# Performance work log

Hardware: AMD Instinct MI355X
Metric: run time of the kernel (lower is better)

Reference implementation:

```python
import jax, jax.numpy as jnp
import numpy as np

OUT, IN = 4096, 4096      # weight_shape
VDIM = 8                  # codebook vector_dim
CODEBOOK_SIZE = 256
LEVEL = 2                 # haar_decomposition_level
INV_SQRT2 = 0.7071067811865476


def unpack_bool(packed, shape):
    # packed: int array of bytes (values 0..255); unpack 8 bits per byte (LSB first)
    bits = (packed[:, None] >> jnp.arange(8, dtype=packed.dtype)) & 1  # [n_bytes, 8]
    return bits.reshape(shape)


def inverse_haar(c, level):
    # c: [..., n] orthonormal Haar coefficients laid out [a_L, d_L, d_{L-1}, ..., d_1]
    n = c.shape[-1]
    m = n >> level
    a = c[..., :m]
    while m < n:
        d = c[..., m:2 * m]
        even = (a + d) * INV_SQRT2
        odd = (a - d) * INV_SQRT2
        a = jnp.stack([even, odd], axis=-1).reshape(c.shape[:-1] + (2 * m,))
        m *= 2
    return a


def setup_inputs() -> dict:
    key = jax.random.key(0)
    k1, k2, k3, k4, k5 = jax.random.split(key, 5)
    x = jax.random.normal(k1, (4, 2048, IN), dtype=jnp.float32)
    codebook = jax.random.normal(k2, (CODEBOOK_SIZE, VDIM), dtype=jnp.float32)
    scales = jax.random.uniform(k5, (OUT, 1), dtype=jnp.float32)
    indices = jax.random.randint(k3, (OUT * IN // VDIM,), 0, CODEBOOK_SIZE, dtype=jnp.int32)
    signs_packed = jax.random.randint(k4, (OUT * IN // 8,), 0, 256, dtype=jnp.int32)
    return {"x": x, "codebook": codebook, "scales": scales,
            "indices": indices, "signs_packed": signs_packed}


def reference(x, codebook, scales, indices, signs_packed):
    # codebook gather -> haar-domain magnitudes, reshaped to signs_shape = weight shape
    haar_freq = codebook[indices].reshape(OUT, IN)
    # unpack sign bits and map {0,1} -> {-1,+1}
    signs = 2.0 * unpack_bool(signs_packed, (OUT, IN)).astype(haar_freq.dtype) - 1.0
    haar_freq = haar_freq * signs
    # multi-level inverse Haar wavelet along in_features
    w = inverse_haar(haar_freq, LEVEL)
    w = w * scales  # per-output-row scales
    return jnp.einsum('bsi,oi->bso', x, w)
```

## Files before the change

### kernel.cpp

```cpp
#include <hip/hip_runtime.h>
#include <hip/hip_bf16.h>

typedef unsigned short u16;
typedef unsigned int u32;
typedef float f32x4 __attribute__((ext_vector_type(4)));
typedef u16 u16x4 __attribute__((ext_vector_type(4)));
typedef u16 u16x8 __attribute__((ext_vector_type(8)));
typedef __bf16 bf16x8 __attribute__((ext_vector_type(8)));

#define OUT_DIM 4096
#define IN_DIM  4096
#define M_DIM   8192

__device__ __forceinline__ u16 f2bf(float f) {
  u32 u = __builtin_bit_cast(u32, f);
  return (u16)((u + 0x7FFFu + ((u >> 16) & 1u)) >> 16);
}

__global__ __launch_bounds__(256) void build_w_kernel(
    const float* __restrict__ codebook, const float* __restrict__ scales,
    const int* __restrict__ indices, const int* __restrict__ signs,
    u16* __restrict__ W) {
  __shared__ float c[IN_DIM];
  const int o   = blockIdx.x;
  const int tid = threadIdx.x;
  for (int g = tid; g < IN_DIM / 8; g += 256) {
    const int idx = indices[o * (IN_DIM / 8) + g];
    const int sp  = signs[o * (IN_DIM / 8) + g];
    f32x4 c0 = *(const f32x4*)&codebook[idx * 8];
    f32x4 c1 = *(const f32x4*)&codebook[idx * 8 + 4];
    float v[8] = {c0[0], c0[1], c0[2], c0[3], c1[0], c1[1], c1[2], c1[3]};
#pragma unroll
    for (int j = 0; j < 8; ++j)
      c[g * 8 + j] = ((sp >> j) & 1) ? v[j] : -v[j];
  }
  __syncthreads();
  const float scale = scales[o];
  const float S = 0.70710678118654752440f;
  for (int t = tid; t < IN_DIM / 4; t += 256) {
    float a   = c[t];
    float d1  = c[IN_DIM / 4 + t];
    float d2a = c[IN_DIM / 2 + 2 * t];
    float d2b = c[IN_DIM / 2 + 2 * t + 1];
    float e  = (a + d1) * S;
    float od = (a - d1) * S;
    u16x4 w;
    w[0] = f2bf((e  + d2a) * S * scale);
    w[1] = f2bf((e  - d2a) * S * scale);
    w[2] = f2bf((od + d2b) * S * scale);
    w[3] = f2bf((od - d2b) * S * scale);
    *(u16x4*)&W[(size_t)o * IN_DIM + 4 * t] = w;
  }
}

__global__ __launch_bounds__(256) void cvt_x_kernel(
    const float* __restrict__ X, u16* __restrict__ Xb) {
  const int stride = gridDim.x * blockDim.x;
  const int n8 = (M_DIM * IN_DIM) / 8;
  for (int i = blockIdx.x * blockDim.x + threadIdx.x; i < n8; i += stride) {
    f32x4 a = *(const f32x4*)&X[(size_t)i * 8];
    f32x4 b = *(const f32x4*)&X[(size_t)i * 8 + 4];
    u16x8 r;
    r[0] = f2bf(a[0]); r[1] = f2bf(a[1]); r[2] = f2bf(a[2]); r[3] = f2bf(a[3]);
    r[4] = f2bf(b[0]); r[5] = f2bf(b[1]); r[6] = f2bf(b[2]); r[7] = f2bf(b[3]);
    *(u16x8*)&Xb[(size_t)i * 8] = r;
  }
}

__global__ __launch_bounds__(512, 1) void gemm_bt_kernel(
    const u16* __restrict__ A,
    const u16* __restrict__ B,
    float*     __restrict__ C) {
  constexpr int K   = IN_DIM;
  constexpr int NT  = K / 64;
  constexpr int NIT = NT / 2;
  extern __shared__ char smem[];

  const int tid  = threadIdx.x;
  const int wave = tid >> 6;
  const int lane = tid & 63;

  const int swz = (blockIdx.x & 7) * 64 + (blockIdx.x >> 3);
  const int bm = (swz >> 4) * 256;
  const int bn = (swz & 15) * 256;

  const int wr  = (wave >> 2) * 128;
  const int wc  = (wave & 3) * 64;
  const int fr  = lane & 15;
  const int fkB = (lane >> 4) * 16;

  int offA[2][4], offB[4];
#pragma unroll
  for (int mq = 0; mq < 2; ++mq)
#pragma unroll
    for (int m = 0; m < 4; ++m) {
      int o = (wr + mq * 64 + m * 16 + fr) * 64 + fkB;
      offA[mq][m] = o ^ ((o >> 3) & 0x30);
    }
#pragma unroll
  for (int n = 0; n < 4; ++n) {
    int o = (wc + n * 16 + fr) * 64 + fkB;
    offB[n] = 16384 + (o ^ ((o >> 3) & 0x30));
  }

  const int d0 = tid * 16,        d1 = 8192 + tid * 16;
  const int l0 = d0 ^ ((d0 >> 3) & 0x30), l1 = d1 ^ ((d1 >> 3) & 0x30);
  const u16* srcA0 = A + (size_t)(bm + (d0 >> 6)) * K + ((l0 & 63) >> 1);
  const u16* srcA1 = A + (size_t)(bm + (d1 >> 6)) * K + ((l1 & 63) >> 1);
  const u16* srcB0 = B + (size_t)(bn + (d0 >> 6)) * K + ((l0 & 63) >> 1);
  const u16* srcB1 = B + (size_t)(bn + (d1 >> 6)) * K + ((l1 & 63) >> 1);
  const int ldsW = wave * 1024;

#define GLD(SRC, DST)                                              \
  __builtin_amdgcn_global_load_lds(                                \
      (const __attribute__((address_space(1))) void*)(SRC),        \
      (__attribute__((address_space(3))) void*)(DST), 16, 0, 0)

  auto stageRegion = [&](int bufi, int ks, int tile) {
    char* base = smem + bufi * 65536 + ks * 32768 + ldsW;
    const u16* a0 = srcA0 + tile * 64 + ks * 32;
    const u16* a1 = srcA1 + tile * 64 + ks * 32;
    const u16* b0 = srcB0 + tile * 64 + ks * 32;
    const u16* b1 = srcB1 + tile * 64 + ks * 32;
    GLD(a0, base);
    GLD(a1, base + 8192);
    GLD(b0, base + 16384);
    GLD(b1, base + 24576);
  };

  f32x4 acc[8][4] = {};
  bf16x8 aq0[4], aq1[4], bq0[4], bq1[4];

#define RD_A(DST, BUFI, KS, MQ)                                              \
  _Pragma("unroll")                                                          \
  for (int m = 0; m < 4; ++m)                                                \
    DST[m] = *(const bf16x8*)(smem + (BUFI) * 65536 + (KS) * 32768 +         \
                              offA[MQ][m]);
#define RD_B(DST, BUFI, KS)                                                  \
  _Pragma("unroll")                                                          \
  for (int n = 0; n < 4; ++n)                                                \
    DST[n] = *(const bf16x8*)(smem + (BUFI) * 65536 + (KS) * 32768 +         \
                              offB[n]);
#define MM(CA, CB, MQ)                                                       \
  __builtin_amdgcn_s_setprio(1);                                             \
  _Pragma("unroll")                                                          \
  for (int m = 0; m < 4; ++m)                                                \
    _Pragma("unroll")                                                        \
    for (int n = 0; n < 4; ++n)                                              \
      acc[(MQ) * 4 + m][n] = __builtin_amdgcn_mfma_f32_16x16x32_bf16(        \
          CA[m], CB[n], acc[(MQ) * 4 + m][n], 0, 0, 0);                      \
  __builtin_amdgcn_s_setprio(0);
#define BAR                                                                  \
  __builtin_amdgcn_sched_barrier(0);                                         \
  __builtin_amdgcn_s_barrier();
#define LG(N) asm volatile("s_waitcnt lgkmcnt(" #N ")" ::: "memory")
#define VM(N) asm volatile("s_waitcnt vmcnt(" #N ")" ::: "memory")

  stageRegion(0, 0, 0);
  stageRegion(0, 1, 0);
  stageRegion(1, 0, 1);
  VM(4);
  __builtin_amdgcn_s_barrier();
  RD_B(bq0, 0, 0)
  RD_A(aq0, 0, 0, 0)

  for (int i = 0; i < NIT - 1; ++i) {
    const int t0 = 2 * i;
    RD_A(aq1, 0, 0, 1)                                  BAR LG(4); MM(aq0, bq0, 0)
    RD_B(bq1, 0, 1) RD_A(aq0, 0, 1, 0)
    stageRegion(1, 1, t0 + 1); VM(4);                   BAR LG(8); MM(aq1, bq0, 1)
    RD_A(aq1, 0, 1, 1)                                  BAR LG(4); MM(aq0, bq1, 0)
    RD_B(bq0, 1, 0) RD_A(aq0, 1, 0, 0)
    stageRegion(0, 0, t0 + 2); VM(4);                   BAR LG(8); MM(aq1, bq1, 1)
    RD_A(aq1, 1, 0, 1)                                  BAR LG(4); MM(aq0, bq0, 0)
    RD_B(bq1, 1, 1) RD_A(aq0, 1, 1, 0)
    stageRegion(0, 1, t0 + 2); VM(4);                   BAR LG(8); MM(aq1, bq0, 1)
    RD_A(aq1, 1, 1, 1)                                  BAR LG(4); MM(aq0, bq1, 0)
    RD_B(bq0, 0, 0) RD_A(aq0, 0, 0, 0)
    stageRegion(1, 0, t0 + 3); VM(4);                   BAR LG(8); MM(aq1, bq1, 1)
  }

  {
    RD_A(aq1, 0, 0, 1)                                  BAR LG(4); MM(aq0, bq0, 0)
    RD_B(bq1, 0, 1) RD_A(aq0, 0, 1, 0)
    stageRegion(1, 1, NT - 1); VM(4);                   BAR LG(8); MM(aq1, bq0, 1)
    RD_A(aq1, 0, 1, 1)                                  BAR LG(4); MM(aq0, bq1, 0)
    RD_B(bq0, 1, 0) RD_A(aq0, 1, 0, 0) VM(0);           BAR LG(8); MM(aq1, bq1, 1)
    RD_A(aq1, 1, 0, 1)                                  BAR LG(4); MM(aq0, bq0, 0)
    RD_B(bq1, 1, 1) RD_A(aq0, 1, 1, 0)                  BAR LG(8); MM(aq1, bq0, 1)
    RD_A(aq1, 1, 1, 1)                                  BAR LG(4); MM(aq0, bq1, 0)
                                                        BAR LG(0); MM(aq1, bq1, 1)
  }
#undef RD_A
#undef RD_B
#undef MM
#undef BAR
#undef LG
#undef VM
#undef GLD

#pragma unroll
  for (int h = 0; h < 8; ++h)
#pragma unroll
    for (int n = 0; n < 4; ++n) {
      const int col = bn + wc + n * 16 + fr;
#pragma unroll
      for (int j = 0; j < 4; ++j) {
        const int row = bm + wr + h * 16 + (lane >> 4) * 4 + j;
        C[(size_t)row * OUT_DIM + col] = acc[h][n][j];
      }
    }
}

extern "C" void kernel_launch(void* const* d_in, const int* in_sizes, int n_in,
                              void* d_out, int out_size, void* d_ws, size_t ws_size,
                              hipStream_t stream) {
  const float* x        = (const float*)d_in[0];
  const float* codebook = (const float*)d_in[1];
  const float* scales   = (const float*)d_in[2];
  const int*   indices  = (const int*)d_in[3];
  const int*   signs    = (const int*)d_in[4];
  float* out = (float*)d_out;

  u16* W  = (u16*)d_ws;
  u16* Xb = (u16*)d_ws + (size_t)OUT_DIM * IN_DIM;

  (void)hipFuncSetAttribute((const void*)gemm_bt_kernel,
                            hipFuncAttributeMaxDynamicSharedMemorySize, 131072);

  build_w_kernel<<<OUT_DIM, 256, 0, stream>>>(codebook, scales, indices, signs, W);
  cvt_x_kernel<<<2048, 256, 0, stream>>>(x, Xb);
  gemm_bt_kernel<<<(M_DIM / 256) * (OUT_DIM / 256), 512, 131072, stream>>>(Xb, W, out);
}
```

Baseline: 292.8 us.

## Fuse fp32-to-bf16 activation conversion into GEMM A-tile staging

Removes the separate kernel that converted X from fp32 to bf16 into a workspace buffer. The GEMM now loads fp32 A tiles into registers, converts them to bf16, and writes them to LDS itself. Only B still uses direct global-to-LDS loads. This drops a full 128 MB read and 64 MB write pass plus one launch. In exchange, each GEMM block reads twice as many bytes for A, and the pipeline moves to single-buffered fragment registers with full lgkmcnt(0) waits, which may reduce latency hiding.

```diff
diff --git a/kernel.cpp b/kernel.cpp
--- a/kernel.cpp
+++ b/kernel.cpp
@@ -53,22 +53,8 @@
   }
 }
 
-__global__ __launch_bounds__(256) void cvt_x_kernel(
-    const float* __restrict__ X, u16* __restrict__ Xb) {
-  const int stride = gridDim.x * blockDim.x;
-  const int n8 = (M_DIM * IN_DIM) / 8;
-  for (int i = blockIdx.x * blockDim.x + threadIdx.x; i < n8; i += stride) {
-    f32x4 a = *(const f32x4*)&X[(size_t)i * 8];
-    f32x4 b = *(const f32x4*)&X[(size_t)i * 8 + 4];
-    u16x8 r;
-    r[0] = f2bf(a[0]); r[1] = f2bf(a[1]); r[2] = f2bf(a[2]); r[3] = f2bf(a[3]);
-    r[4] = f2bf(b[0]); r[5] = f2bf(b[1]); r[6] = f2bf(b[2]); r[7] = f2bf(b[3]);
-    *(u16x8*)&Xb[(size_t)i * 8] = r;
-  }
-}
-
 __global__ __launch_bounds__(512, 1) void gemm_bt_kernel(
-    const u16* __restrict__ A,
+    const float* __restrict__ X,
     const u16* __restrict__ B,
     float*     __restrict__ C) {
   constexpr int K   = IN_DIM;
@@ -105,8 +91,8 @@
 
   const int d0 = tid * 16,        d1 = 8192 + tid * 16;
   const int l0 = d0 ^ ((d0 >> 3) & 0x30), l1 = d1 ^ ((d1 >> 3) & 0x30);
-  const u16* srcA0 = A + (size_t)(bm + (d0 >> 6)) * K + ((l0 & 63) >> 1);
-  const u16* srcA1 = A + (size_t)(bm + (d1 >> 6)) * K + ((l1 & 63) >> 1);
+  const float* srcAf0 = X + (size_t)(bm + (d0 >> 6)) * K + ((l0 & 63) >> 1);
+  const float* srcAf1 = X + (size_t)(bm + (d1 >> 6)) * K + ((l1 & 63) >> 1);
   const u16* srcB0 = B + (size_t)(bn + (d0 >> 6)) * K + ((l0 & 63) >> 1);
   const u16* srcB1 = B + (size_t)(bn + (d1 >> 6)) * K + ((l1 & 63) >> 1);
   const int ldsW = wave * 1024;
@@ -116,87 +102,109 @@
       (const __attribute__((address_space(1))) void*)(SRC),        \
       (__attribute__((address_space(3))) void*)(DST), 16, 0, 0)
 
-  auto stageRegion = [&](int bufi, int ks, int tile) {
-    char* base = smem + bufi * 65536 + ks * 32768 + ldsW;
-    const u16* a0 = srcA0 + tile * 64 + ks * 32;
-    const u16* a1 = srcA1 + tile * 64 + ks * 32;
+  auto bgld = [&](int bufi, int ks, int tile) {
+    char* base = smem + bufi * 65536 + ks * 32768 + 16384 + ldsW;
     const u16* b0 = srcB0 + tile * 64 + ks * 32;
     const u16* b1 = srcB1 + tile * 64 + ks * 32;
-    GLD(a0, base);
-    GLD(a1, base + 8192);
-    GLD(b0, base + 16384);
-    GLD(b1, base + 24576);
+    GLD(b0, base);
+    GLD(b1, base + 8192);
   };
 
   f32x4 acc[8][4] = {};
-  bf16x8 aq0[4], aq1[4], bq0[4], bq1[4];
-
-#define RD_A(DST, BUFI, KS, MQ)                                              \
+  bf16x8 aq[4], bq[4];
+  f32x4 areg[4];
+
+#define ALOAD(KS, TILE)                                                      \
+  {                                                                          \
+    const float* pa = srcAf0 + (TILE) * 64 + (KS) * 32;                      \
+    const float* pb = srcAf1 + (TILE) * 64 + (KS) * 32;                      \
+    areg[0] = *(const f32x4*)pa;                                             \
+    areg[1] = *(const f32x4*)(pa + 4);                                       \
+    areg[2] = *(const f32x4*)pb;                                             \
+    areg[3] = *(const f32x4*)(pb + 4);                                       \
+  }
+
+#define AWRITE(BUFI, KS)                                                     \
+  {                                                                          \
+    u16x8 w0, w1;                                                            \
+    _Pragma("unroll")                                                        \
+    for (int e = 0; e < 4; ++e) {                                            \
+      w0[e]     = __builtin_bit_cast(u16, (__bf16)areg[0][e]);               \
+      w0[4 + e] = __builtin_bit_cast(u16, (__bf16)areg[1][e]);               \
+      w1[e]     = __builtin_bit_cast(u16, (__bf16)areg[2][e]);               \
+      w1[4 + e] = __builtin_bit_cast(u16, (__bf16)areg[3][e]);               \
+    }                                                                        \
+    *(u16x8*)(smem + (BUFI) * 65536 + (KS) * 32768 + d0) = w0;               \
+    *(u16x8*)(smem + (BUFI) * 65536 + (KS) * 32768 + d1) = w1;               \
+  }
+
+#define RD_B(BUFI, KS)                                                       \
+  _Pragma("unroll")                                                          \
+  for (int n = 0; n < 4; ++n)                                                \
+    bq[n] = *(const bf16x8*)(smem + (BUFI) * 65536 + (KS) * 32768 + offB[n]);
+#define RD_A(BUFI, KS, MQ)                                                   \
   _Pragma("unroll")                                                          \
   for (int m = 0; m < 4; ++m)                                                \
-    DST[m] = *(const bf16x8*)(smem + (BUFI) * 65536 + (KS) * 32768 +         \
-                              offA[MQ][m]);
-#define RD_B(DST, BUFI, KS)                                                  \
-  _Pragma("unroll")                                                          \
-  for (int n = 0; n < 4; ++n)                                                \
-    DST[n] = *(const bf16x8*)(smem + (BUFI) * 65536 + (KS) * 32768 +         \
-                              offB[n]);
-#define MM(CA, CB, MQ)                                                       \
+    aq[m] = *(const bf16x8*)(smem + (BUFI) * 65536 + (KS) * 32768 +          \
+                             offA[MQ][m]);
+#define MM(MQ)                                                               \
   __builtin_amdgcn_s_setprio(1);                                             \
   _Pragma("unroll")                                                          \
   for (int m = 0; m < 4; ++m)                                                \
     _Pragma("unroll")                                                        \
     for (int n = 0; n < 4; ++n)                                              \
       acc[(MQ) * 4 + m][n] = __builtin_amdgcn_mfma_f32_16x16x32_bf16(        \
-          CA[m], CB[n], acc[(MQ) * 4 + m][n], 0, 0, 0);                      \
+          aq[m], bq[n], acc[(MQ) * 4 + m][n], 0, 0, 0);                      \
   __builtin_amdgcn_s_setprio(0);
-#define BAR                                                                  \
-  __builtin_amdgcn_sched_barrier(0);                                         \
-  __builtin_amdgcn_s_barrier();
-#define LG(N) asm volatile("s_waitcnt lgkmcnt(" #N ")" ::: "memory")
-#define VM(N) asm volatile("s_waitcnt vmcnt(" #N ")" ::: "memory")
-
-  stageRegion(0, 0, 0);
-  stageRegion(0, 1, 0);
-  stageRegion(1, 0, 1);
-  VM(4);
-  __builtin_amdgcn_s_barrier();
-  RD_B(bq0, 0, 0)
-  RD_A(aq0, 0, 0, 0)
+#define BARM asm volatile("s_barrier" ::: "memory")
+#define LG0  asm volatile("s_waitcnt lgkmcnt(0)" ::: "memory")
+#define VM0  asm volatile("s_waitcnt vmcnt(0)" ::: "memory")
+#define VM6  asm volatile("s_waitcnt vmcnt(6)" ::: "memory")
+
+#define PHODD(BUFI, KS)                                                      \
+  RD_B(BUFI, KS) RD_A(BUFI, KS, 0) BARM; LG0; MM(0)
+#define PHEVEN(BUFI, KS, PRE, POST)                                          \
+  RD_A(BUFI, KS, 1) PRE POST LG0; BARM; MM(1)
+
+  ALOAD(0, 0) AWRITE(0, 0)
+  ALOAD(1, 0) AWRITE(0, 1)
+  ALOAD(0, 1) AWRITE(1, 0)
+  bgld(0, 0, 0); bgld(0, 1, 0); bgld(1, 0, 1);
+  ALOAD(1, 1)
+  VM6; LG0; BARM;
 
   for (int i = 0; i < NIT - 1; ++i) {
     const int t0 = 2 * i;
-    RD_A(aq1, 0, 0, 1)                                  BAR LG(4); MM(aq0, bq0, 0)
-    RD_B(bq1, 0, 1) RD_A(aq0, 0, 1, 0)
-    stageRegion(1, 1, t0 + 1); VM(4);                   BAR LG(8); MM(aq1, bq0, 1)
-    RD_A(aq1, 0, 1, 1)                                  BAR LG(4); MM(aq0, bq1, 0)
-    RD_B(bq0, 1, 0) RD_A(aq0, 1, 0, 0)
-    stageRegion(0, 0, t0 + 2); VM(4);                   BAR LG(8); MM(aq1, bq1, 1)
-    RD_A(aq1, 1, 0, 1)                                  BAR LG(4); MM(aq0, bq0, 0)
-    RD_B(bq1, 1, 1) RD_A(aq0, 1, 1, 0)
-    stageRegion(0, 1, t0 + 2); VM(4);                   BAR LG(8); MM(aq1, bq0, 1)
-    RD_A(aq1, 1, 1, 1)                                  BAR LG(4); MM(aq0, bq1, 0)
-    RD_B(bq0, 0, 0) RD_A(aq0, 0, 0, 0)
-    stageRegion(1, 0, t0 + 3); VM(4);                   BAR LG(8); MM(aq1, bq1, 1)
-  }
-
-  {
-    RD_A(aq1, 0, 0, 1)                                  BAR LG(4); MM(aq0, bq0, 0)
-    RD_B(bq1, 0, 1) RD_A(aq0, 0, 1, 0)
-    stageRegion(1, 1, NT - 1); VM(4);                   BAR LG(8); MM(aq1, bq0, 1)
-    RD_A(aq1, 0, 1, 1)                                  BAR LG(4); MM(aq0, bq1, 0)
-    RD_B(bq0, 1, 0) RD_A(aq0, 1, 0, 0) VM(0);           BAR LG(8); MM(aq1, bq1, 1)
-    RD_A(aq1, 1, 0, 1)                                  BAR LG(4); MM(aq0, bq0, 0)
-    RD_B(bq1, 1, 1) RD_A(aq0, 1, 1, 0)                  BAR LG(8); MM(aq1, bq0, 1)
-    RD_A(aq1, 1, 1, 1)                                  BAR LG(4); MM(aq0, bq1, 0)
-                                                        BAR LG(0); MM(aq1, bq1, 1)
-  }
+    PHODD (0, 0)
+    PHEVEN(0, 0, AWRITE(1, 1), bgld(1, 1, t0 + 1); ALOAD(0, t0 + 2))
+    PHODD (0, 1)
+    PHEVEN(0, 1, AWRITE(0, 0), bgld(0, 0, t0 + 2); ALOAD(1, t0 + 2))
+    PHODD (1, 0)
+    PHEVEN(1, 0, AWRITE(0, 1), bgld(0, 1, t0 + 2); ALOAD(0, t0 + 3))
+    PHODD (1, 1)
+    PHEVEN(1, 1, AWRITE(1, 0), bgld(1, 0, t0 + 3); ALOAD(1, t0 + 3))
+  }
+
+  PHODD (0, 0)
+  PHEVEN(0, 0, AWRITE(1, 1), bgld(1, 1, NT - 1);)
+  PHODD (0, 1)
+  PHEVEN(0, 1, , VM0;)
+  PHODD (1, 0)
+  PHEVEN(1, 0, , )
+  PHODD (1, 1)
+  PHEVEN(1, 1, , )
+
+#undef PHODD
+#undef PHEVEN
 #undef RD_A
 #undef RD_B
 #undef MM
-#undef BAR
-#undef LG
-#undef VM
+#undef BARM
+#undef LG0
+#undef VM0
+#undef VM6
+#undef ALOAD
+#undef AWRITE
 #undef GLD
 
 #pragma unroll
@@ -222,13 +230,11 @@
   const int*   signs    = (const int*)d_in[4];
   float* out = (float*)d_out;
 
-  u16* W  = (u16*)d_ws;
-  u16* Xb = (u16*)d_ws + (size_t)OUT_DIM * IN_DIM;
+  u16* W = (u16*)d_ws;
 
   (void)hipFuncSetAttribute((const void*)gemm_bt_kernel,
                             hipFuncAttributeMaxDynamicSharedMemorySize, 131072);
 
   build_w_kernel<<<OUT_DIM, 256, 0, stream>>>(codebook, scales, indices, signs, W);
-  cvt_x_kernel<<<2048, 256, 0, stream>>>(x, Xb);
-  gemm_bt_kernel<<<(M_DIM / 256) * (OUT_DIM / 256), 512, 131072, stream>>>(Xb, W, out);
-}
+  gemm_bt_kernel<<<(M_DIM / 256) * (OUT_DIM / 256), 512, 131072, stream>>>(x, W, out);
+}
```

After: 463.1 us. 58.2% more time.
